# Kernel optimization log

Hardware: AMD Instinct MI355X
Metric: run time of the kernel (lower is better)

Reference implementation:

```python
import jax, jax.numpy as jnp
import numpy as np

# Canonical topology: root object with K arrays, each array has L number leaves.
# Weights are tied across paths (tie_weights_containers=tie_weights_primitives=True),
# NumberEmbedder runs in eval mode with initial buffers mean=0, sqmean=1 -> identity norm.

K, L, D = 8192, 128, 64


def setup_inputs() -> dict:
    key = jax.random.key(0)
    ks = jax.random.split(key, 16)
    s = 1.0 / np.sqrt(D)
    return {
        "x": jax.random.normal(ks[0], (K, L), dtype=jnp.float32),
        "W_num": jax.random.normal(ks[1], (D, 1), dtype=jnp.float32) * s,
        "b_num": jax.random.normal(ks[2], (D,), dtype=jnp.float32) * s,
        "W_ih": jax.random.normal(ks[3], (4 * D, 2 * D), dtype=jnp.float32) * s,
        "W_hh": jax.random.normal(ks[4], (4 * D, D), dtype=jnp.float32) * s,
        "b_ih": jax.random.normal(ks[5], (4 * D,), dtype=jnp.float32) * s,
        "b_hh": jax.random.normal(ks[6], (4 * D,), dtype=jnp.float32) * s,
        "W_aout": jax.random.normal(ks[7], (D, D), dtype=jnp.float32) * s,
        "b_aout": jax.random.normal(ks[8], (D,), dtype=jnp.float32) * s,
        "W_fh": jax.random.normal(ks[9], (D, D), dtype=jnp.float32) * s,
        "b_fh": jax.random.normal(ks[10], (D,), dtype=jnp.float32) * s,
        "W_iouh": jax.random.normal(ks[11], (3 * D, D), dtype=jnp.float32) * s,
        "b_iouh": jax.random.normal(ks[12], (3 * D,), dtype=jnp.float32) * s,
        "W_oout": jax.random.normal(ks[13], (D, D), dtype=jnp.float32) * s,
        "b_oout": jax.random.normal(ks[14], (D,), dtype=jnp.float32) * s,
    }


def _forward(x, W_num, b_num, W_ih, W_hh, b_ih, b_hh, W_aout, b_aout,
             W_fh, b_fh, W_iouh, b_iouh, W_oout, b_oout):
    d = W_hh.shape[1]
    # --- NumberEmbedder: Linear(1, d) on identity-normalized numbers; c = 0 ---
    emb = x[..., None] * W_num[:, 0] + b_num          # [K, L, d]
    xs = jnp.transpose(emb, (1, 0, 2))                # [L, K, d] time-major for scan
    # --- ArrayEmbedder: LSTMCell over children; input = cat(child_h, child_c) ---
    # child_c is identically zero, so only the first half of W_ih contributes.
    W_ih_h = W_ih[:, :d]                              # [4d, d]
    bias = b_ih + b_hh                                # [4d]

    def step(carry, x_t):
        h, c = carry
        gates = x_t @ W_ih_h.T + h @ W_hh.T + bias    # [K, 4d]
        i, f, g, o = jnp.split(gates, 4, axis=1)
        c2 = jax.nn.sigmoid(f) * c + jax.nn.sigmoid(i) * jnp.tanh(g)
        h2 = jax.nn.sigmoid(o) * jnp.tanh(c2)
        return (h2, c2), None

    h0 = jnp.zeros((x.shape[0], d), dtype=x.dtype)
    (h_arr, c_arr), _ = jax.lax.scan(step, (h0, h0), xs)
    h_hat = h_arr @ W_aout.T + b_aout                 # [K, d] array lout
    # --- ObjectEmbedder: child-sum TreeLSTM over the K array states ---
    f = h_hat @ W_fh.T + b_fh                         # [K, d]
    fc_sum = jnp.sum(jax.nn.sigmoid(f) * c_arr, axis=0, keepdims=True)  # [1, d]
    hs_bar = jnp.sum(h_hat, axis=0, keepdims=True)    # [1, d]
    iou = hs_bar @ W_iouh.T + b_iouh                  # [1, 3d]
    i, o, u = jnp.split(iou, 3, axis=1)
    c_obj = jax.nn.sigmoid(i) * jnp.tanh(u) + fc_sum
    h_obj = jax.nn.sigmoid(o) * jnp.tanh(c_obj)
    h_hat_obj = h_obj @ W_oout.T + b_oout             # [1, d] object lout
    # root forward returns cat(h, c)
    return jnp.concatenate([h_hat_obj, c_obj], axis=1)  # [1, 2d]


def reference(x, W_num, b_num, W_ih, W_hh, b_ih, b_hh, W_aout, b_aout,
              W_fh, b_fh, W_iouh, b_iouh, W_oout, b_oout):
    return _forward(x, W_num, b_num, W_ih, W_hh, b_ih, b_hh, W_aout, b_aout,
                    W_fh, b_fh, W_iouh, b_iouh, W_oout, b_oout)
```

## Files before the change

### kernel.cpp

```cpp
#include <hip/hip_runtime.h>
#include <cstddef>

#define D   64
#define L   128
#define NT  256
#define ROWS 16
#define XSS 132
#define HBS 72
#define NBLK 512
#define LOG2E 1.4426950408889634f

typedef __attribute__((ext_vector_type(8))) short short8;
typedef __attribute__((ext_vector_type(4))) float floatx4;
typedef __attribute__((ext_vector_type(2))) float f2;

__device__ __forceinline__ float fast_rcp(float x) {
#if defined(__has_builtin)
#if __has_builtin(__builtin_amdgcn_rcpf)
  return __builtin_amdgcn_rcpf(x);
#else
  return 1.0f / x;
#endif
#else
  return 1.0f / x;
#endif
}
__device__ __forceinline__ float ex2(float x) {
#if defined(__has_builtin)
#if __has_builtin(__builtin_amdgcn_exp2f)
  return __builtin_amdgcn_exp2f(x);
#else
  return __builtin_exp2f(x);
#endif
#else
  return __builtin_exp2f(x);
#endif
}
__device__ __forceinline__ f2 ex2_2(f2 v) { return (f2){ex2(v.x), ex2(v.y)}; }
__device__ __forceinline__ f2 rcp_2(f2 v) { return (f2){fast_rcp(v.x), fast_rcp(v.y)}; }
__device__ __forceinline__ float sig_plain(float x) {
  return fast_rcp(1.0f + ex2(-LOG2E * x));
}
__device__ __forceinline__ float tanh2(float G) {
  return fmaf(2.0f, fast_rcp(1.0f + ex2(G)), -1.0f);
}
__device__ __forceinline__ unsigned short f2bf_rtne(float f) {
  unsigned int u = __float_as_uint(f);
  u += 0x7fffu + ((u >> 16) & 1u);
  return (unsigned short)(u >> 16);
}
__device__ __forceinline__ float bf2f(unsigned short s) {
  return __uint_as_float(((unsigned int)s) << 16);
}

__global__ __launch_bounds__(NT, 2)
void lstm_main(const float* __restrict__ x,
               const float* __restrict__ W_num,
               const float* __restrict__ b_num,
               const float* __restrict__ W_ih,
               const float* __restrict__ W_hh,
               const float* __restrict__ b_ih,
               const float* __restrict__ b_hh,
               const float* __restrict__ W_aout,
               const float* __restrict__ b_aout,
               const float* __restrict__ W_fh,
               const float* __restrict__ b_fh,
               const float* __restrict__ W_iouh,
               const float* __restrict__ b_iouh,
               const float* __restrict__ W_oout,
               const float* __restrict__ b_oout,
               float* __restrict__ acc_out,
               float* __restrict__ out)
{
  __shared__ __align__(16) float xs[ROWS * XSS];
  __shared__ __align__(16) short hb[2][ROWS * HBS];
  __shared__ float sacc[2 * D];
  __shared__ float hobj[D];
  __shared__ int   is_last;

  const int tid  = threadIdx.x;
  const int w    = tid >> 6;
  const int lane = tid & 63;
  const int quad = lane >> 4;
  const int c16  = lane & 15;
  const int k0   = blockIdx.x * ROWS;
  const int dcol = w * 16 + c16;

  for (int i = tid; i < ROWS * (L / 4); i += NT) {
    int r = i >> 5, c4 = i & 31;
    float4 v = ((const float4*)(x + (size_t)(k0 + r) * L))[c4];
    float* dst = &xs[r * XSS + c4 * 4];
    dst[0] = v.x; dst[1] = v.y; dst[2] = v.z; dst[3] = v.w;
  }
  for (int i = tid; i < ROWS * HBS; i += NT) hb[0][i] = 0;

  const float gscale[4] = {-LOG2E, -LOG2E, -2.0f * LOG2E, -LOG2E};

  float An[4], Bc[4];
#pragma unroll
  for (int g = 0; g < 4; ++g) {
    int j = g * 64 + dcol;
    const float4* wr = (const float4*)(W_ih + (size_t)j * (2 * D));
    float a = 0.0f, b = b_ih[j] + b_hh[j];
#pragma unroll
    for (int e4 = 0; e4 < 16; ++e4) {
      float4 wv = wr[e4];
      float4 wn = ((const float4*)W_num)[e4];
      float4 bn = ((const float4*)b_num)[e4];
      a = fmaf(wn.x, wv.x, a); a = fmaf(wn.y, wv.y, a);
      a = fmaf(wn.z, wv.z, a); a = fmaf(wn.w, wv.w, a);
      b = fmaf(bn.x, wv.x, b); b = fmaf(bn.y, wv.y, b);
      b = fmaf(bn.z, wv.z, b); b = fmaf(bn.w, wv.w, b);
    }
    An[g] = a * gscale[g]; Bc[g] = b * gscale[g];
  }

  short8 Bf[4][2];
#pragma unroll
  for (int g = 0; g < 4; ++g) {
#pragma unroll
    for (int kk = 0; kk < 2; ++kk) {
      const float4* wp = (const float4*)(W_hh + (size_t)(g * 64 + dcol) * D
                                         + kk * 32 + quad * 8);
      float wv[8];
      float4 w0 = wp[0], w1 = wp[1];
      wv[0]=w0.x; wv[1]=w0.y; wv[2]=w0.z; wv[3]=w0.w;
      wv[4]=w1.x; wv[5]=w1.y; wv[6]=w1.z; wv[7]=w1.w;
      short8 hi8;
#pragma unroll
      for (int j = 0; j < 8; ++j)
        hi8[j] = (short)f2bf_rtne(wv[j] * gscale[g]);
      Bf[g][kk] = hi8;
    }
  }

  const f2 one2  = {1.0f, 1.0f};
  const f2 m2l2  = {-2.0f * LOG2E, -2.0f * LOG2E};
  f2 creg2[2] = {{0.f, 0.f}, {0.f, 0.f}};
  f2 hreg2[2] = {{0.f, 0.f}, {0.f, 0.f}};
  __syncthreads();

  int p = 0;
  for (int t4 = 0; t4 < L; t4 += 4) {
    float4 xq[4];
#pragma unroll
    for (int r = 0; r < 4; ++r)
      xq[r] = *(const float4*)&xs[(quad * 4 + r) * XSS + t4];
#pragma unroll
    for (int u = 0; u < 4; ++u) {
      short8 ahi[2];
#pragma unroll
      for (int kk = 0; kk < 2; ++kk)
        ahi[kk] = *(const short8*)&hb[p][c16 * HBS + kk * 32 + quad * 8];
      f2 xv01 = {xq[0][u], xq[1][u]};
      f2 xv23 = {xq[2][u], xq[3][u]};
      floatx4 acc[4];
#pragma unroll
      for (int g = 0; g < 4; ++g) {
        f2 A2 = {An[g], An[g]}, B2 = {Bc[g], Bc[g]};
        f2 i01 = A2 * xv01 + B2;
        f2 i23 = A2 * xv23 + B2;
        acc[g] = (floatx4){i01.x, i01.y, i23.x, i23.y};
      }
#pragma unroll
      for (int kk = 0; kk < 2; ++kk) {
#pragma unroll
        for (int g = 0; g < 4; ++g)
          acc[g] = __builtin_amdgcn_mfma_f32_16x16x32_bf16(ahi[kk], Bf[g][kk], acc[g], 0, 0, 0);
      }
#pragma unroll
      for (int h = 0; h < 2; ++h) {
        f2 Gi = {acc[0][2*h], acc[0][2*h+1]};
        f2 Gf = {acc[1][2*h], acc[1][2*h+1]};
        f2 Gg = {acc[2][2*h], acc[2][2*h+1]};
        f2 Go = {acc[3][2*h], acc[3][2*h+1]};
        f2 Ei = ex2_2(Gi), Ef = ex2_2(Gf), Eg = ex2_2(Gg), Eo = ex2_2(Go);
        f2 pf = Ef + one2, pi = Ei + one2, pg = Eg + one2, mg = one2 - Eg;
        f2 pig = pi * pg;
        f2 num = creg2[h] * pig + mg * pf;
        f2 c2  = num * rcp_2(pf * pig);
        creg2[h] = c2;
        f2 Ec = ex2_2(c2 * m2l2);
        f2 po = Eo + one2, pc = Ec + one2, mc = one2 - Ec;
        f2 h2 = mc * rcp_2(po * pc);
        hreg2[h] = h2;
        int row0 = quad * 4 + 2 * h;
        hb[p ^ 1][row0 * HBS + dcol]       = (short)f2bf_rtne(h2.x);
        hb[p ^ 1][(row0 + 1) * HBS + dcol] = (short)f2bf_rtne(h2.y);
      }
      __syncthreads();
      p ^= 1;
    }
  }

  float creg[4] = {creg2[0].x, creg2[0].y, creg2[1].x, creg2[1].y};
  float hreg[4] = {hreg2[0].x, hreg2[0].y, hreg2[1].x, hreg2[1].y};

#pragma unroll
  for (int r = 0; r < 4; ++r) xs[(quad * 4 + r) * XSS + dcol] = hreg[r];
  __syncthreads();

  float hhat[4];
#pragma unroll
  for (int r = 0; r < 4; ++r) {
    float a = b_aout[dcol];
    const float4* wa = (const float4*)(W_aout + (size_t)dcol * D);
    const float* hp = &xs[(quad * 4 + r) * XSS];
#pragma unroll
    for (int e4 = 0; e4 < 16; ++e4) {
      float4 wv = wa[e4];
      a = fmaf(wv.x, hp[e4*4+0], a); a = fmaf(wv.y, hp[e4*4+1], a);
      a = fmaf(wv.z, hp[e4*4+2], a); a = fmaf(wv.w, hp[e4*4+3], a);
    }
    hhat[r] = a;
  }
  __syncthreads();
#pragma unroll
  for (int r = 0; r < 4; ++r) xs[(quad * 4 + r) * XSS + 64 + dcol] = hhat[r];
  __syncthreads();

  float pfc = 0.0f, phs = 0.0f;
#pragma unroll
  for (int r = 0; r < 4; ++r) {
    float f = b_fh[dcol];
    const float4* wf = (const float4*)(W_fh + (size_t)dcol * D);
    const float* hp = &xs[(quad * 4 + r) * XSS + 64];
#pragma unroll
    for (int e4 = 0; e4 < 16; ++e4) {
      float4 wv = wf[e4];
      f = fmaf(wv.x, hp[e4*4+0], f); f = fmaf(wv.y, hp[e4*4+1], f);
      f = fmaf(wv.z, hp[e4*4+2], f); f = fmaf(wv.w, hp[e4*4+3], f);
    }
    pfc = fmaf(sig_plain(f), creg[r], pfc);
    phs += hhat[r];
  }
  pfc += __shfl_xor(pfc, 16); pfc += __shfl_xor(pfc, 32);
  phs += __shfl_xor(phs, 16); phs += __shfl_xor(phs, 32);
  if (quad == 0) {
    atomicAdd(acc_out + dcol, pfc);
    atomicAdd(acc_out + D + dcol, phs);
  }

  __threadfence();
  if (tid == 0) {
    unsigned int prev = __hip_atomic_fetch_add((unsigned int*)(acc_out + 2 * D), 1u,
                                               __ATOMIC_ACQ_REL, __HIP_MEMORY_SCOPE_AGENT);
    is_last = (prev == NBLK - 1) ? 1 : 0;
  }
  __syncthreads();
  if (!is_last) return;
  __threadfence();
  if (tid < 2 * D)
    sacc[tid] = __hip_atomic_load(acc_out + tid, __ATOMIC_RELAXED, __HIP_MEMORY_SCOPE_AGENT);
  __syncthreads();
  if (tid < D) {
    const int d = tid;
    float vi = b_iouh[d], vo = b_iouh[D + d], vu = b_iouh[2 * D + d];
    for (int e = 0; e < D; ++e) {
      float hs = sacc[D + e];
      vi = fmaf(W_iouh[(size_t)d * D + e],           hs, vi);
      vo = fmaf(W_iouh[(size_t)(D + d) * D + e],     hs, vo);
      vu = fmaf(W_iouh[(size_t)(2 * D + d) * D + e], hs, vu);
    }
    float c_obj = sig_plain(vi) * tanh2(-2.0f * LOG2E * vu) + sacc[d];
    float h_obj = sig_plain(vo) * tanh2(-2.0f * LOG2E * c_obj);
    hobj[d] = h_obj;
    out[D + d] = c_obj;
  }
  __syncthreads();
  if (tid < D) {
    const int d = tid;
    float hh = b_oout[d];
    for (int e = 0; e < D; ++e) hh = fmaf(W_oout[(size_t)d * D + e], hobj[e], hh);
    out[d] = hh;
  }
}

extern "C" void kernel_launch(void* const* d_in, const int* in_sizes, int n_in,
                              void* d_out, int out_size, void* d_ws, size_t ws_size,
                              hipStream_t stream) {
  const float* x      = (const float*)d_in[0];
  const float* W_num  = (const float*)d_in[1];
  const float* b_num  = (const float*)d_in[2];
  const float* W_ih   = (const float*)d_in[3];
  const float* W_hh   = (const float*)d_in[4];
  const float* b_ih   = (const float*)d_in[5];
  const float* b_hh   = (const float*)d_in[6];
  const float* W_aout = (const float*)d_in[7];
  const float* b_aout = (const float*)d_in[8];
  const float* W_fh   = (const float*)d_in[9];
  const float* b_fh   = (const float*)d_in[10];
  const float* W_iouh = (const float*)d_in[11];
  const float* b_iouh = (const float*)d_in[12];
  const float* W_oout = (const float*)d_in[13];
  const float* b_oout = (const float*)d_in[14];
  float* acc = (float*)d_ws;
  float* out = (float*)d_out;

  hipMemsetAsync(d_ws, 0, (2 * D + 1) * sizeof(float), stream);
  lstm_main<<<NBLK, NT, 0, stream>>>(x, W_num, b_num, W_ih, W_hh, b_ih, b_hh,
                                     W_aout, b_aout, W_fh, b_fh,
                                     W_iouh, b_iouh, W_oout, b_oout, acc, out);
}
```

Baseline: 202.3 us.

## Halve block to two waves, each computing two 16-column tiles

The block shrinks from 256 to 128 threads, so each wave now owns 32 hidden columns instead of 16. It keeps twice the W_hh fragments and accumulators and issues 8 independent MFMAs per k-slice. The aim is to make each per-timestep __syncthreads cheaper with fewer waves, and to raise instruction-level parallelism so MFMA and transcendental latency in the serial recurrence is hidden. In exchange each wave carries more registers and serial elementwise work. Occupancy per SIMD may also change, so latency hiding across waves could drop.

```diff
diff --git a/kernel.cpp b/kernel.cpp
--- a/kernel.cpp
+++ b/kernel.cpp
@@ -3,7 +3,7 @@
 
 #define D   64
 #define L   128
-#define NT  256
+#define NT  128
 #define ROWS 16
 #define XSS 132
 #define HBS 72
@@ -53,7 +53,7 @@
   return __uint_as_float(((unsigned int)s) << 16);
 }
 
-__global__ __launch_bounds__(NT, 2)
+__global__ __launch_bounds__(NT, 1)
 void lstm_main(const float* __restrict__ x,
                const float* __restrict__ W_num,
                const float* __restrict__ b_num,
@@ -84,7 +84,6 @@
   const int quad = lane >> 4;
   const int c16  = lane & 15;
   const int k0   = blockIdx.x * ROWS;
-  const int dcol = w * 16 + c16;
 
   for (int i = tid; i < ROWS * (L / 4); i += NT) {
     int r = i >> 5, c4 = i & 31;
@@ -96,48 +95,55 @@
 
   const float gscale[4] = {-LOG2E, -LOG2E, -2.0f * LOG2E, -LOG2E};
 
-  float An[4], Bc[4];
-#pragma unroll
-  for (int g = 0; g < 4; ++g) {
-    int j = g * 64 + dcol;
-    const float4* wr = (const float4*)(W_ih + (size_t)j * (2 * D));
-    float a = 0.0f, b = b_ih[j] + b_hh[j];
-#pragma unroll
-    for (int e4 = 0; e4 < 16; ++e4) {
-      float4 wv = wr[e4];
-      float4 wn = ((const float4*)W_num)[e4];
-      float4 bn = ((const float4*)b_num)[e4];
-      a = fmaf(wn.x, wv.x, a); a = fmaf(wn.y, wv.y, a);
-      a = fmaf(wn.z, wv.z, a); a = fmaf(wn.w, wv.w, a);
-      b = fmaf(bn.x, wv.x, b); b = fmaf(bn.y, wv.y, b);
-      b = fmaf(bn.z, wv.z, b); b = fmaf(bn.w, wv.w, b);
-    }
-    An[g] = a * gscale[g]; Bc[g] = b * gscale[g];
-  }
-
-  short8 Bf[4][2];
-#pragma unroll
-  for (int g = 0; g < 4; ++g) {
-#pragma unroll
-    for (int kk = 0; kk < 2; ++kk) {
-      const float4* wp = (const float4*)(W_hh + (size_t)(g * 64 + dcol) * D
-                                         + kk * 32 + quad * 8);
-      float wv[8];
-      float4 w0 = wp[0], w1 = wp[1];
-      wv[0]=w0.x; wv[1]=w0.y; wv[2]=w0.z; wv[3]=w0.w;
-      wv[4]=w1.x; wv[5]=w1.y; wv[6]=w1.z; wv[7]=w1.w;
-      short8 hi8;
-#pragma unroll
-      for (int j = 0; j < 8; ++j)
-        hi8[j] = (short)f2bf_rtne(wv[j] * gscale[g]);
-      Bf[g][kk] = hi8;
+  float An[2][4], Bc[2][4];
+#pragma unroll
+  for (int ct = 0; ct < 2; ++ct) {
+#pragma unroll
+    for (int g = 0; g < 4; ++g) {
+      int j = g * 64 + w * 32 + ct * 16 + c16;
+      const float4* wr = (const float4*)(W_ih + (size_t)j * (2 * D));
+      float a = 0.0f, b = b_ih[j] + b_hh[j];
+#pragma unroll
+      for (int e4 = 0; e4 < 16; ++e4) {
+        float4 wv = wr[e4];
+        float4 wn = ((const float4*)W_num)[e4];
+        float4 bn = ((const float4*)b_num)[e4];
+        a = fmaf(wn.x, wv.x, a); a = fmaf(wn.y, wv.y, a);
+        a = fmaf(wn.z, wv.z, a); a = fmaf(wn.w, wv.w, a);
+        b = fmaf(bn.x, wv.x, b); b = fmaf(bn.y, wv.y, b);
+        b = fmaf(bn.z, wv.z, b); b = fmaf(bn.w, wv.w, b);
+      }
+      An[ct][g] = a * gscale[g]; Bc[ct][g] = b * gscale[g];
+    }
+  }
+
+  short8 Bf[2][4][2];
+#pragma unroll
+  for (int ct = 0; ct < 2; ++ct) {
+#pragma unroll
+    for (int g = 0; g < 4; ++g) {
+#pragma unroll
+      for (int kk = 0; kk < 2; ++kk) {
+        const float4* wp = (const float4*)(W_hh
+                           + (size_t)(g * 64 + w * 32 + ct * 16 + c16) * D
+                           + kk * 32 + quad * 8);
+        float wv[8];
+        float4 w0 = wp[0], w1 = wp[1];
+        wv[0]=w0.x; wv[1]=w0.y; wv[2]=w0.z; wv[3]=w0.w;
+        wv[4]=w1.x; wv[5]=w1.y; wv[6]=w1.z; wv[7]=w1.w;
+        short8 hi8;
+#pragma unroll
+        for (int j = 0; j < 8; ++j)
+          hi8[j] = (short)f2bf_rtne(wv[j] * gscale[g]);
+        Bf[ct][g][kk] = hi8;
+      }
     }
   }
 
   const f2 one2  = {1.0f, 1.0f};
   const f2 m2l2  = {-2.0f * LOG2E, -2.0f * LOG2E};
-  f2 creg2[2] = {{0.f, 0.f}, {0.f, 0.f}};
-  f2 hreg2[2] = {{0.f, 0.f}, {0.f, 0.f}};
+  f2 creg2[2][2] = {{{0.f,0.f},{0.f,0.f}}, {{0.f,0.f},{0.f,0.f}}};
+  f2 hreg2[2][2] = {{{0.f,0.f},{0.f,0.f}}, {{0.f,0.f},{0.f,0.f}}};
   __syncthreads();
 
   int p = 0;
@@ -154,91 +160,131 @@
         ahi[kk] = *(const short8*)&hb[p][c16 * HBS + kk * 32 + quad * 8];
       f2 xv01 = {xq[0][u], xq[1][u]};
       f2 xv23 = {xq[2][u], xq[3][u]};
-      floatx4 acc[4];
-#pragma unroll
-      for (int g = 0; g < 4; ++g) {
-        f2 A2 = {An[g], An[g]}, B2 = {Bc[g], Bc[g]};
-        f2 i01 = A2 * xv01 + B2;
-        f2 i23 = A2 * xv23 + B2;
-        acc[g] = (floatx4){i01.x, i01.y, i23.x, i23.y};
+      floatx4 acc[2][4];
+#pragma unroll
+      for (int ct = 0; ct < 2; ++ct) {
+#pragma unroll
+        for (int g = 0; g < 4; ++g) {
+          f2 A2 = {An[ct][g], An[ct][g]}, B2 = {Bc[ct][g], Bc[ct][g]};
+          f2 i01 = A2 * xv01 + B2;
+          f2 i23 = A2 * xv23 + B2;
+          acc[ct][g] = (floatx4){i01.x, i01.y, i23.x, i23.y};
+        }
       }
 #pragma unroll
       for (int kk = 0; kk < 2; ++kk) {
 #pragma unroll
-        for (int g = 0; g < 4; ++g)
-          acc[g] = __builtin_amdgcn_mfma_f32_16x16x32_bf16(ahi[kk], Bf[g][kk], acc[g], 0, 0, 0);
-      }
-#pragma unroll
-      for (int h = 0; h < 2; ++h) {
-        f2 Gi = {acc[0][2*h], acc[0][2*h+1]};
-        f2 Gf = {acc[1][2*h], acc[1][2*h+1]};
-        f2 Gg = {acc[2][2*h], acc[2][2*h+1]};
-        f2 Go = {acc[3][2*h], acc[3][2*h+1]};
-        f2 Ei = ex2_2(Gi), Ef = ex2_2(Gf), Eg = ex2_2(Gg), Eo = ex2_2(Go);
-        f2 pf = Ef + one2, pi = Ei + one2, pg = Eg + one2, mg = one2 - Eg;
-        f2 pig = pi * pg;
-        f2 num = creg2[h] * pig + mg * pf;
-        f2 c2  = num * rcp_2(pf * pig);
-        creg2[h] = c2;
-        f2 Ec = ex2_2(c2 * m2l2);
-        f2 po = Eo + one2, pc = Ec + one2, mc = one2 - Ec;
-        f2 h2 = mc * rcp_2(po * pc);
-        hreg2[h] = h2;
-        int row0 = quad * 4 + 2 * h;
-        hb[p ^ 1][row0 * HBS + dcol]       = (short)f2bf_rtne(h2.x);
-        hb[p ^ 1][(row0 + 1) * HBS + dcol] = (short)f2bf_rtne(h2.y);
+        for (int ct = 0; ct < 2; ++ct) {
+#pragma unroll
+          for (int g = 0; g < 4; ++g)
+            acc[ct][g] = __builtin_amdgcn_mfma_f32_16x16x32_bf16(
+                           ahi[kk], Bf[ct][g][kk], acc[ct][g], 0, 0, 0);
+        }
+      }
+#pragma unroll
+      for (int ct = 0; ct < 2; ++ct) {
+        const int dcol = w * 32 + ct * 16 + c16;
+#pragma unroll
+        for (int h = 0; h < 2; ++h) {
+          f2 Gi = {acc[ct][0][2*h], acc[ct][0][2*h+1]};
+          f2 Gf = {acc[ct][1][2*h], acc[ct][1][2*h+1]};
+          f2 Gg = {acc[ct][2][2*h], acc[ct][2][2*h+1]};
+          f2 Go = {acc[ct][3][2*h], acc[ct][3][2*h+1]};
+          f2 Ei = ex2_2(Gi), Ef = ex2_2(Gf), Eg = ex2_2(Gg), Eo = ex2_2(Go);
+          f2 pf = Ef + one2, pi = Ei + one2, pg = Eg + one2, mg = one2 - Eg;
+          f2 pig = pi * pg;
+          f2 num = creg2[ct][h] * pig + mg * pf;
+          f2 c2  = num * rcp_2(pf * pig);
+          creg2[ct][h] = c2;
+          f2 Ec = ex2_2(c2 * m2l2);
+          f2 po = Eo + one2, pc = Ec + one2, mc = one2 - Ec;
+          f2 h2 = mc * rcp_2(po * pc);
+          hreg2[ct][h] = h2;
+          int row0 = quad * 4 + 2 * h;
+          hb[p ^ 1][row0 * HBS + dcol]       = (short)f2bf_rtne(h2.x);
+          hb[p ^ 1][(row0 + 1) * HBS + dcol] = (short)f2bf_rtne(h2.y);
+        }
       }
       __syncthreads();
       p ^= 1;
     }
   }
 
-  float creg[4] = {creg2[0].x, creg2[0].y, creg2[1].x, creg2[1].y};
-  float hreg[4] = {hreg2[0].x, hreg2[0].y, hreg2[1].x, hreg2[1].y};
-
-#pragma unroll
-  for (int r = 0; r < 4; ++r) xs[(quad * 4 + r) * XSS + dcol] = hreg[r];
-  __syncthreads();
-
-  float hhat[4];
-#pragma unroll
-  for (int r = 0; r < 4; ++r) {
-    float a = b_aout[dcol];
-    const float4* wa = (const float4*)(W_aout + (size_t)dcol * D);
-    const float* hp = &xs[(quad * 4 + r) * XSS];
-#pragma unroll
-    for (int e4 = 0; e4 < 16; ++e4) {
-      float4 wv = wa[e4];
-      a = fmaf(wv.x, hp[e4*4+0], a); a = fmaf(wv.y, hp[e4*4+1], a);
-      a = fmaf(wv.z, hp[e4*4+2], a); a = fmaf(wv.w, hp[e4*4+3], a);
-    }
-    hhat[r] = a;
-  }
-  __syncthreads();
-#pragma unroll
-  for (int r = 0; r < 4; ++r) xs[(quad * 4 + r) * XSS + 64 + dcol] = hhat[r];
-  __syncthreads();
-
-  float pfc = 0.0f, phs = 0.0f;
-#pragma unroll
-  for (int r = 0; r < 4; ++r) {
-    float f = b_fh[dcol];
-    const float4* wf = (const float4*)(W_fh + (size_t)dcol * D);
-    const float* hp = &xs[(quad * 4 + r) * XSS + 64];
-#pragma unroll
-    for (int e4 = 0; e4 < 16; ++e4) {
-      float4 wv = wf[e4];
-      f = fmaf(wv.x, hp[e4*4+0], f); f = fmaf(wv.y, hp[e4*4+1], f);
-      f = fmaf(wv.z, hp[e4*4+2], f); f = fmaf(wv.w, hp[e4*4+3], f);
-    }
-    pfc = fmaf(sig_plain(f), creg[r], pfc);
-    phs += hhat[r];
-  }
-  pfc += __shfl_xor(pfc, 16); pfc += __shfl_xor(pfc, 32);
-  phs += __shfl_xor(phs, 16); phs += __shfl_xor(phs, 32);
+  float creg[2][4], hreg[2][4];
+#pragma unroll
+  for (int ct = 0; ct < 2; ++ct) {
+    creg[ct][0] = creg2[ct][0].x; creg[ct][1] = creg2[ct][0].y;
+    creg[ct][2] = creg2[ct][1].x; creg[ct][3] = creg2[ct][1].y;
+    hreg[ct][0] = hreg2[ct][0].x; hreg[ct][1] = hreg2[ct][0].y;
+    hreg[ct][2] = hreg2[ct][1].x; hreg[ct][3] = hreg2[ct][1].y;
+  }
+
+#pragma unroll
+  for (int ct = 0; ct < 2; ++ct) {
+    const int dcol = w * 32 + ct * 16 + c16;
+#pragma unroll
+    for (int r = 0; r < 4; ++r) xs[(quad * 4 + r) * XSS + dcol] = hreg[ct][r];
+  }
+  __syncthreads();
+
+  float hhat[2][4];
+#pragma unroll
+  for (int ct = 0; ct < 2; ++ct) {
+    const int dcol = w * 32 + ct * 16 + c16;
+#pragma unroll
+    for (int r = 0; r < 4; ++r) {
+      float a = b_aout[dcol];
+      const float4* wa = (const float4*)(W_aout + (size_t)dcol * D);
+      const float* hp = &xs[(quad * 4 + r) * XSS];
+#pragma unroll
+      for (int e4 = 0; e4 < 16; ++e4) {
+        float4 wv = wa[e4];
+        a = fmaf(wv.x, hp[e4*4+0], a); a = fmaf(wv.y, hp[e4*4+1], a);
+        a = fmaf(wv.z, hp[e4*4+2], a); a = fmaf(wv.w, hp[e4*4+3], a);
+      }
+      hhat[ct][r] = a;
+    }
+  }
+  __syncthreads();
+#pragma unroll
+  for (int ct = 0; ct < 2; ++ct) {
+    const int dcol = w * 32 + ct * 16 + c16;
+#pragma unroll
+    for (int r = 0; r < 4; ++r) xs[(quad * 4 + r) * XSS + 64 + dcol] = hhat[ct][r];
+  }
+  __syncthreads();
+
+  float pfc[2] = {0.0f, 0.0f}, phs[2] = {0.0f, 0.0f};
+#pragma unroll
+  for (int ct = 0; ct < 2; ++ct) {
+    const int dcol = w * 32 + ct * 16 + c16;
+#pragma unroll
+    for (int r = 0; r < 4; ++r) {
+      float f = b_fh[dcol];
+      const float4* wf = (const float4*)(W_fh + (size_t)dcol * D);
+      const float* hp = &xs[(quad * 4 + r) * XSS + 64];
+#pragma unroll
+      for (int e4 = 0; e4 < 16; ++e4) {
+        float4 wv = wf[e4];
+        f = fmaf(wv.x, hp[e4*4+0], f); f = fmaf(wv.y, hp[e4*4+1], f);
+        f = fmaf(wv.z, hp[e4*4+2], f); f = fmaf(wv.w, hp[e4*4+3], f);
+      }
+      pfc[ct] = fmaf(sig_plain(f), creg[ct][r], pfc[ct]);
+      phs[ct] += hhat[ct][r];
+    }
+  }
+#pragma unroll
+  for (int ct = 0; ct < 2; ++ct) {
+    pfc[ct] += __shfl_xor(pfc[ct], 16); pfc[ct] += __shfl_xor(pfc[ct], 32);
+    phs[ct] += __shfl_xor(phs[ct], 16); phs[ct] += __shfl_xor(phs[ct], 32);
+  }
   if (quad == 0) {
-    atomicAdd(acc_out + dcol, pfc);
-    atomicAdd(acc_out + D + dcol, phs);
+#pragma unroll
+    for (int ct = 0; ct < 2; ++ct) {
+      const int dcol = w * 32 + ct * 16 + c16;
+      atomicAdd(acc_out + dcol, pfc[ct]);
+      atomicAdd(acc_out + D + dcol, phs[ct]);
+    }
   }
 
   __threadfence();
```

New measurement: 224.5 us. +11.0%, slower.

## Process two interleaved 16-row tiles per block to hide recurrent latency

Applied to the files above, without the earlier changes.

Each block now handles 32 rows as two independent 16-row LSTM tiles, interleaving their MFMA and transcendental work within each timestep and sharing one barrier per step. The grid halves to 256 blocks and launch bounds drop to one block per SIMD slot. The aim is to fill the serial dependency chain of each recurrence with independent work and amortise barrier cost. In exchange, register pressure rises and the 256-block grid may underfill the GPU's compute units.

```diff
diff --git a/kernel.cpp b/kernel.cpp
--- a/kernel.cpp
+++ b/kernel.cpp
@@ -4,10 +4,11 @@
 #define D   64
 #define L   128
 #define NT  256
-#define ROWS 16
+#define TR  16
+#define ROWS 32
 #define XSS 132
 #define HBS 72
-#define NBLK 512
+#define NBLK 256
 #define LOG2E 1.4426950408889634f
 
 typedef __attribute__((ext_vector_type(8))) short short8;
@@ -49,11 +50,8 @@
   u += 0x7fffu + ((u >> 16) & 1u);
   return (unsigned short)(u >> 16);
 }
-__device__ __forceinline__ float bf2f(unsigned short s) {
-  return __uint_as_float(((unsigned int)s) << 16);
-}
-
-__global__ __launch_bounds__(NT, 2)
+
+__global__ __launch_bounds__(NT, 1)
 void lstm_main(const float* __restrict__ x,
                const float* __restrict__ W_num,
                const float* __restrict__ b_num,
@@ -73,7 +71,7 @@
                float* __restrict__ out)
 {
   __shared__ __align__(16) float xs[ROWS * XSS];
-  __shared__ __align__(16) short hb[2][ROWS * HBS];
+  __shared__ __align__(16) short hb[2][2][TR * HBS];
   __shared__ float sacc[2 * D];
   __shared__ float hobj[D];
   __shared__ int   is_last;
@@ -92,7 +90,7 @@
     float* dst = &xs[r * XSS + c4 * 4];
     dst[0] = v.x; dst[1] = v.y; dst[2] = v.z; dst[3] = v.w;
   }
-  for (int i = tid; i < ROWS * HBS; i += NT) hb[0][i] = 0;
+  for (int i = tid; i < 2 * 2 * TR * HBS; i += NT) ((short*)hb)[i] = 0;
 
   const float gscale[4] = {-LOG2E, -LOG2E, -2.0f * LOG2E, -LOG2E};
 
@@ -136,103 +134,135 @@
 
   const f2 one2  = {1.0f, 1.0f};
   const f2 m2l2  = {-2.0f * LOG2E, -2.0f * LOG2E};
-  f2 creg2[2] = {{0.f, 0.f}, {0.f, 0.f}};
-  f2 hreg2[2] = {{0.f, 0.f}, {0.f, 0.f}};
-  __syncthreads();
+  f2 cregA[2] = {{0.f, 0.f}, {0.f, 0.f}};
+  f2 hregA[2] = {{0.f, 0.f}, {0.f, 0.f}};
+  f2 cregB[2] = {{0.f, 0.f}, {0.f, 0.f}};
+  f2 hregB[2] = {{0.f, 0.f}, {0.f, 0.f}};
+  __syncthreads();
+
+  auto cell_step = [&](const short8 ahi[2], f2 creg2[2], f2 hreg2[2],
+                       f2 xv01, f2 xv23, short* hbw) {
+    floatx4 acc[4];
+#pragma unroll
+    for (int g = 0; g < 4; ++g) {
+      f2 A2 = {An[g], An[g]}, B2 = {Bc[g], Bc[g]};
+      f2 i01 = A2 * xv01 + B2;
+      f2 i23 = A2 * xv23 + B2;
+      acc[g] = (floatx4){i01.x, i01.y, i23.x, i23.y};
+    }
+#pragma unroll
+    for (int kk = 0; kk < 2; ++kk) {
+#pragma unroll
+      for (int g = 0; g < 4; ++g)
+        acc[g] = __builtin_amdgcn_mfma_f32_16x16x32_bf16(ahi[kk], Bf[g][kk], acc[g], 0, 0, 0);
+    }
+#pragma unroll
+    for (int h = 0; h < 2; ++h) {
+      f2 Gi = {acc[0][2*h], acc[0][2*h+1]};
+      f2 Gf = {acc[1][2*h], acc[1][2*h+1]};
+      f2 Gg = {acc[2][2*h], acc[2][2*h+1]};
+      f2 Go = {acc[3][2*h], acc[3][2*h+1]};
+      f2 Ei = ex2_2(Gi), Ef = ex2_2(Gf), Eg = ex2_2(Gg), Eo = ex2_2(Go);
+      f2 pf = Ef + one2, pi = Ei + one2, pg = Eg + one2, mg = one2 - Eg;
+      f2 pig = pi * pg;
+      f2 num = creg2[h] * pig + mg * pf;
+      f2 c2  = num * rcp_2(pf * pig);
+      creg2[h] = c2;
+      f2 Ec = ex2_2(c2 * m2l2);
+      f2 po = Eo + one2, pc = Ec + one2, mc = one2 - Ec;
+      f2 h2 = mc * rcp_2(po * pc);
+      hreg2[h] = h2;
+      int row0 = quad * 4 + 2 * h;
+      hbw[row0 * HBS + dcol]       = (short)f2bf_rtne(h2.x);
+      hbw[(row0 + 1) * HBS + dcol] = (short)f2bf_rtne(h2.y);
+    }
+  };
 
   int p = 0;
   for (int t4 = 0; t4 < L; t4 += 4) {
-    float4 xq[4];
-#pragma unroll
-    for (int r = 0; r < 4; ++r)
-      xq[r] = *(const float4*)&xs[(quad * 4 + r) * XSS + t4];
+    float4 xqA[4], xqB[4];
+#pragma unroll
+    for (int r = 0; r < 4; ++r) {
+      xqA[r] = *(const float4*)&xs[(quad * 4 + r) * XSS + t4];
+      xqB[r] = *(const float4*)&xs[(TR + quad * 4 + r) * XSS + t4];
+    }
 #pragma unroll
     for (int u = 0; u < 4; ++u) {
-      short8 ahi[2];
+      short8 aA[2], aB[2];
 #pragma unroll
       for (int kk = 0; kk < 2; ++kk)
-        ahi[kk] = *(const short8*)&hb[p][c16 * HBS + kk * 32 + quad * 8];
-      f2 xv01 = {xq[0][u], xq[1][u]};
-      f2 xv23 = {xq[2][u], xq[3][u]};
-      floatx4 acc[4];
-#pragma unroll
-      for (int g = 0; g < 4; ++g) {
-        f2 A2 = {An[g], An[g]}, B2 = {Bc[g], Bc[g]};
-        f2 i01 = A2 * xv01 + B2;
-        f2 i23 = A2 * xv23 + B2;
-        acc[g] = (floatx4){i01.x, i01.y, i23.x, i23.y};
-      }
-#pragma unroll
-      for (int kk = 0; kk < 2; ++kk) {
-#pragma unroll
-        for (int g = 0; g < 4; ++g)
-          acc[g] = __builtin_amdgcn_mfma_f32_16x16x32_bf16(ahi[kk], Bf[g][kk], acc[g], 0, 0, 0);
-      }
-#pragma unroll
-      for (int h = 0; h < 2; ++h) {
-        f2 Gi = {acc[0][2*h], acc[0][2*h+1]};
-        f2 Gf = {acc[1][2*h], acc[1][2*h+1]};
-        f2 Gg = {acc[2][2*h], acc[2][2*h+1]};
-        f2 Go = {acc[3][2*h], acc[3][2*h+1]};
-        f2 Ei = ex2_2(Gi), Ef = ex2_2(Gf), Eg = ex2_2(Gg), Eo = ex2_2(Go);
-        f2 pf = Ef + one2, pi = Ei + one2, pg = Eg + one2, mg = one2 - Eg;
-        f2 pig = pi * pg;
-        f2 num = creg2[h] * pig + mg * pf;
-        f2 c2  = num * rcp_2(pf * pig);
-        creg2[h] = c2;
-        f2 Ec = ex2_2(c2 * m2l2);
-        f2 po = Eo + one2, pc = Ec + one2, mc = one2 - Ec;
-        f2 h2 = mc * rcp_2(po * pc);
-        hreg2[h] = h2;
-        int row0 = quad * 4 + 2 * h;
-        hb[p ^ 1][row0 * HBS + dcol]       = (short)f2bf_rtne(h2.x);
-        hb[p ^ 1][(row0 + 1) * HBS + dcol] = (short)f2bf_rtne(h2.y);
-      }
+        aA[kk] = *(const short8*)&hb[0][p][c16 * HBS + kk * 32 + quad * 8];
+#pragma unroll
+      for (int kk = 0; kk < 2; ++kk)
+        aB[kk] = *(const short8*)&hb[1][p][c16 * HBS + kk * 32 + quad * 8];
+
+      f2 xA01 = {xqA[0][u], xqA[1][u]};
+      f2 xA23 = {xqA[2][u], xqA[3][u]};
+      cell_step(aA, cregA, hregA, xA01, xA23, &hb[0][p ^ 1][0]);
+
+      f2 xB01 = {xqB[0][u], xqB[1][u]};
+      f2 xB23 = {xqB[2][u], xqB[3][u]};
+      cell_step(aB, cregB, hregB, xB01, xB23, &hb[1][p ^ 1][0]);
+
       __syncthreads();
       p ^= 1;
     }
   }
 
-  float creg[4] = {creg2[0].x, creg2[0].y, creg2[1].x, creg2[1].y};
-  float hreg[4] = {hreg2[0].x, hreg2[0].y, hreg2[1].x, hreg2[1].y};
-
-#pragma unroll
-  for (int r = 0; r < 4; ++r) xs[(quad * 4 + r) * XSS + dcol] = hreg[r];
-  __syncthreads();
-
-  float hhat[4];
-#pragma unroll
-  for (int r = 0; r < 4; ++r) {
-    float a = b_aout[dcol];
-    const float4* wa = (const float4*)(W_aout + (size_t)dcol * D);
-    const float* hp = &xs[(quad * 4 + r) * XSS];
-#pragma unroll
-    for (int e4 = 0; e4 < 16; ++e4) {
-      float4 wv = wa[e4];
-      a = fmaf(wv.x, hp[e4*4+0], a); a = fmaf(wv.y, hp[e4*4+1], a);
-      a = fmaf(wv.z, hp[e4*4+2], a); a = fmaf(wv.w, hp[e4*4+3], a);
-    }
-    hhat[r] = a;
-  }
-  __syncthreads();
-#pragma unroll
-  for (int r = 0; r < 4; ++r) xs[(quad * 4 + r) * XSS + 64 + dcol] = hhat[r];
+  float creg[2][4] = {{cregA[0].x, cregA[0].y, cregA[1].x, cregA[1].y},
+                      {cregB[0].x, cregB[0].y, cregB[1].x, cregB[1].y}};
+  float hreg[2][4] = {{hregA[0].x, hregA[0].y, hregA[1].x, hregA[1].y},
+                      {hregB[0].x, hregB[0].y, hregB[1].x, hregB[1].y}};
+
+#pragma unroll
+  for (int s = 0; s < 2; ++s)
+#pragma unroll
+    for (int r = 0; r < 4; ++r)
+      xs[(s * TR + quad * 4 + r) * XSS + dcol] = hreg[s][r];
+  __syncthreads();
+
+  float hhat[2][4];
+#pragma unroll
+  for (int s = 0; s < 2; ++s) {
+#pragma unroll
+    for (int r = 0; r < 4; ++r) {
+      float a = b_aout[dcol];
+      const float4* wa = (const float4*)(W_aout + (size_t)dcol * D);
+      const float* hp = &xs[(s * TR + quad * 4 + r) * XSS];
+#pragma unroll
+      for (int e4 = 0; e4 < 16; ++e4) {
+        float4 wv = wa[e4];
+        a = fmaf(wv.x, hp[e4*4+0], a); a = fmaf(wv.y, hp[e4*4+1], a);
+        a = fmaf(wv.z, hp[e4*4+2], a); a = fmaf(wv.w, hp[e4*4+3], a);
+      }
+      hhat[s][r] = a;
+    }
+  }
+  __syncthreads();
+#pragma unroll
+  for (int s = 0; s < 2; ++s)
+#pragma unroll
+    for (int r = 0; r < 4; ++r)
+      xs[(s * TR + quad * 4 + r) * XSS + 64 + dcol] = hhat[s][r];
   __syncthreads();
 
   float pfc = 0.0f, phs = 0.0f;
 #pragma unroll
-  for (int r = 0; r < 4; ++r) {
-    float f = b_fh[dcol];
-    const float4* wf = (const float4*)(W_fh + (size_t)dcol * D);
-    const float* hp = &xs[(quad * 4 + r) * XSS + 64];
-#pragma unroll
-    for (int e4 = 0; e4 < 16; ++e4) {
-      float4 wv = wf[e4];
-      f = fmaf(wv.x, hp[e4*4+0], f); f = fmaf(wv.y, hp[e4*4+1], f);
-      f = fmaf(wv.z, hp[e4*4+2], f); f = fmaf(wv.w, hp[e4*4+3], f);
-    }
-    pfc = fmaf(sig_plain(f), creg[r], pfc);
-    phs += hhat[r];
+  for (int s = 0; s < 2; ++s) {
+#pragma unroll
+    for (int r = 0; r < 4; ++r) {
+      float f = b_fh[dcol];
+      const float4* wf = (const float4*)(W_fh + (size_t)dcol * D);
+      const float* hp = &xs[(s * TR + quad * 4 + r) * XSS + 64];
+#pragma unroll
+      for (int e4 = 0; e4 < 16; ++e4) {
+        float4 wv = wf[e4];
+        f = fmaf(wv.x, hp[e4*4+0], f); f = fmaf(wv.y, hp[e4*4+1], f);
+        f = fmaf(wv.z, hp[e4*4+2], f); f = fmaf(wv.w, hp[e4*4+3], f);
+      }
+      pfc = fmaf(sig_plain(f), creg[s][r], pfc);
+      phs += hhat[s][r];
+    }
   }
   pfc += __shfl_xor(pfc, 16); pfc += __shfl_xor(pfc, 32);
   phs += __shfl_xor(phs, 16); phs += __shfl_xor(phs, 32);
```

Result: slower. 221.3 us (+9.4%).

## Run each 16-row LSTM tile in a single wavefront without per-step barriers

Applied to the files above, without the earlier changes.

Shrinks the block from four waves to one wave that computes all 64 hidden columns (16 MFMA tiles per k-chunk) for its 16 rows. Because only one wave touches the hidden-state buffer, the per-timestep __syncthreads and the double-buffered hb are dropped, and hidden states are written with packed 64-bit LDS stores. The epilogue matvecs and reductions are restructured so each lane handles four columns. In exchange, each wave does four times as much serial MFMA and transcendental work per step. With 512 single-wave blocks, fewer SIMDs per CU may have work to hide latency, and register pressure rises.

```diff
diff --git a/kernel.cpp b/kernel.cpp
--- a/kernel.cpp
+++ b/kernel.cpp
@@ -3,7 +3,7 @@
 
 #define D   64
 #define L   128
-#define NT  256
+#define NT  64
 #define ROWS 16
 #define XSS 132
 #define HBS 72
@@ -49,11 +49,8 @@
   u += 0x7fffu + ((u >> 16) & 1u);
   return (unsigned short)(u >> 16);
 }
-__device__ __forceinline__ float bf2f(unsigned short s) {
-  return __uint_as_float(((unsigned int)s) << 16);
-}
-
-__global__ __launch_bounds__(NT, 2)
+
+__global__ __launch_bounds__(NT, 1)
 void lstm_main(const float* __restrict__ x,
                const float* __restrict__ W_num,
                const float* __restrict__ b_num,
@@ -73,18 +70,16 @@
                float* __restrict__ out)
 {
   __shared__ __align__(16) float xs[ROWS * XSS];
-  __shared__ __align__(16) short hb[2][ROWS * HBS];
+  __shared__ __align__(16) short hb[ROWS * HBS];
   __shared__ float sacc[2 * D];
   __shared__ float hobj[D];
   __shared__ int   is_last;
 
   const int tid  = threadIdx.x;
-  const int w    = tid >> 6;
-  const int lane = tid & 63;
-  const int quad = lane >> 4;
-  const int c16  = lane & 15;
+  const int quad = tid >> 4;
+  const int c16  = tid & 15;
   const int k0   = blockIdx.x * ROWS;
-  const int dcol = w * 16 + c16;
+  const int col0 = 4 * c16;
 
   for (int i = tid; i < ROWS * (L / 4); i += NT) {
     int r = i >> 5, c4 = i & 31;
@@ -92,36 +87,41 @@
     float* dst = &xs[r * XSS + c4 * 4];
     dst[0] = v.x; dst[1] = v.y; dst[2] = v.z; dst[3] = v.w;
   }
-  for (int i = tid; i < ROWS * HBS; i += NT) hb[0][i] = 0;
+  for (int i = tid; i < ROWS * HBS; i += NT) hb[i] = 0;
 
   const float gscale[4] = {-LOG2E, -LOG2E, -2.0f * LOG2E, -LOG2E};
 
-  float An[4], Bc[4];
-#pragma unroll
-  for (int g = 0; g < 4; ++g) {
-    int j = g * 64 + dcol;
+  float4 wn[16], bn[16];
+#pragma unroll
+  for (int e4 = 0; e4 < 16; ++e4) {
+    wn[e4] = ((const float4*)W_num)[e4];
+    bn[e4] = ((const float4*)b_num)[e4];
+  }
+
+  float An[16], Bc[16];
+#pragma unroll
+  for (int t = 0; t < 16; ++t) {
+    int j = (t >> 2) * 64 + col0 + (t & 3);
     const float4* wr = (const float4*)(W_ih + (size_t)j * (2 * D));
     float a = 0.0f, b = b_ih[j] + b_hh[j];
 #pragma unroll
     for (int e4 = 0; e4 < 16; ++e4) {
       float4 wv = wr[e4];
-      float4 wn = ((const float4*)W_num)[e4];
-      float4 bn = ((const float4*)b_num)[e4];
-      a = fmaf(wn.x, wv.x, a); a = fmaf(wn.y, wv.y, a);
-      a = fmaf(wn.z, wv.z, a); a = fmaf(wn.w, wv.w, a);
-      b = fmaf(bn.x, wv.x, b); b = fmaf(bn.y, wv.y, b);
-      b = fmaf(bn.z, wv.z, b); b = fmaf(bn.w, wv.w, b);
-    }
-    An[g] = a * gscale[g]; Bc[g] = b * gscale[g];
-  }
-
-  short8 Bf[4][2];
-#pragma unroll
-  for (int g = 0; g < 4; ++g) {
+      a = fmaf(wn[e4].x, wv.x, a); a = fmaf(wn[e4].y, wv.y, a);
+      a = fmaf(wn[e4].z, wv.z, a); a = fmaf(wn[e4].w, wv.w, a);
+      b = fmaf(bn[e4].x, wv.x, b); b = fmaf(bn[e4].y, wv.y, b);
+      b = fmaf(bn[e4].z, wv.z, b); b = fmaf(bn[e4].w, wv.w, b);
+    }
+    An[t] = a * gscale[t >> 2]; Bc[t] = b * gscale[t >> 2];
+  }
+
+  short8 Bf[16][2];
+#pragma unroll
+  for (int t = 0; t < 16; ++t) {
 #pragma unroll
     for (int kk = 0; kk < 2; ++kk) {
-      const float4* wp = (const float4*)(W_hh + (size_t)(g * 64 + dcol) * D
-                                         + kk * 32 + quad * 8);
+      const float4* wp = (const float4*)(W_hh
+          + (size_t)((t >> 2) * 64 + col0 + (t & 3)) * D + kk * 32 + quad * 8);
       float wv[8];
       float4 w0 = wp[0], w1 = wp[1];
       wv[0]=w0.x; wv[1]=w0.y; wv[2]=w0.z; wv[3]=w0.w;
@@ -129,18 +129,19 @@
       short8 hi8;
 #pragma unroll
       for (int j = 0; j < 8; ++j)
-        hi8[j] = (short)f2bf_rtne(wv[j] * gscale[g]);
-      Bf[g][kk] = hi8;
-    }
-  }
-
-  const f2 one2  = {1.0f, 1.0f};
-  const f2 m2l2  = {-2.0f * LOG2E, -2.0f * LOG2E};
-  f2 creg2[2] = {{0.f, 0.f}, {0.f, 0.f}};
-  f2 hreg2[2] = {{0.f, 0.f}, {0.f, 0.f}};
-  __syncthreads();
-
-  int p = 0;
+        hi8[j] = (short)f2bf_rtne(wv[j] * gscale[t >> 2]);
+      Bf[t][kk] = hi8;
+    }
+  }
+
+  const f2 one2 = {1.0f, 1.0f};
+  const f2 m2l2 = {-2.0f * LOG2E, -2.0f * LOG2E};
+  f2 creg2[4][2] = {{{0.f,0.f},{0.f,0.f}}, {{0.f,0.f},{0.f,0.f}},
+                    {{0.f,0.f},{0.f,0.f}}, {{0.f,0.f},{0.f,0.f}}};
+  f2 hreg2[4][2] = {{{0.f,0.f},{0.f,0.f}}, {{0.f,0.f},{0.f,0.f}},
+                    {{0.f,0.f},{0.f,0.f}}, {{0.f,0.f},{0.f,0.f}}};
+  __syncthreads();
+
   for (int t4 = 0; t4 < L; t4 += 4) {
     float4 xq[4];
 #pragma unroll
@@ -151,94 +152,125 @@
       short8 ahi[2];
 #pragma unroll
       for (int kk = 0; kk < 2; ++kk)
-        ahi[kk] = *(const short8*)&hb[p][c16 * HBS + kk * 32 + quad * 8];
+        ahi[kk] = *(const short8*)&hb[c16 * HBS + kk * 32 + quad * 8];
       f2 xv01 = {xq[0][u], xq[1][u]};
       f2 xv23 = {xq[2][u], xq[3][u]};
-      floatx4 acc[4];
-#pragma unroll
-      for (int g = 0; g < 4; ++g) {
-        f2 A2 = {An[g], An[g]}, B2 = {Bc[g], Bc[g]};
+      floatx4 acc[16];
+#pragma unroll
+      for (int t = 0; t < 16; ++t) {
+        f2 A2 = {An[t], An[t]}, B2 = {Bc[t], Bc[t]};
         f2 i01 = A2 * xv01 + B2;
         f2 i23 = A2 * xv23 + B2;
-        acc[g] = (floatx4){i01.x, i01.y, i23.x, i23.y};
+        acc[t] = (floatx4){i01.x, i01.y, i23.x, i23.y};
       }
 #pragma unroll
       for (int kk = 0; kk < 2; ++kk) {
 #pragma unroll
-        for (int g = 0; g < 4; ++g)
-          acc[g] = __builtin_amdgcn_mfma_f32_16x16x32_bf16(ahi[kk], Bf[g][kk], acc[g], 0, 0, 0);
-      }
-#pragma unroll
-      for (int h = 0; h < 2; ++h) {
-        f2 Gi = {acc[0][2*h], acc[0][2*h+1]};
-        f2 Gf = {acc[1][2*h], acc[1][2*h+1]};
-        f2 Gg = {acc[2][2*h], acc[2][2*h+1]};
-        f2 Go = {acc[3][2*h], acc[3][2*h+1]};
-        f2 Ei = ex2_2(Gi), Ef = ex2_2(Gf), Eg = ex2_2(Gg), Eo = ex2_2(Go);
-        f2 pf = Ef + one2, pi = Ei + one2, pg = Eg + one2, mg = one2 - Eg;
-        f2 pig = pi * pg;
-        f2 num = creg2[h] * pig + mg * pf;
-        f2 c2  = num * rcp_2(pf * pig);
-        creg2[h] = c2;
-        f2 Ec = ex2_2(c2 * m2l2);
-        f2 po = Eo + one2, pc = Ec + one2, mc = one2 - Ec;
-        f2 h2 = mc * rcp_2(po * pc);
-        hreg2[h] = h2;
-        int row0 = quad * 4 + 2 * h;
-        hb[p ^ 1][row0 * HBS + dcol]       = (short)f2bf_rtne(h2.x);
-        hb[p ^ 1][(row0 + 1) * HBS + dcol] = (short)f2bf_rtne(h2.y);
-      }
-      __syncthreads();
-      p ^= 1;
-    }
-  }
-
-  float creg[4] = {creg2[0].x, creg2[0].y, creg2[1].x, creg2[1].y};
-  float hreg[4] = {hreg2[0].x, hreg2[0].y, hreg2[1].x, hreg2[1].y};
-
-#pragma unroll
-  for (int r = 0; r < 4; ++r) xs[(quad * 4 + r) * XSS + dcol] = hreg[r];
-  __syncthreads();
-
-  float hhat[4];
+        for (int t = 0; t < 16; ++t)
+          acc[t] = __builtin_amdgcn_mfma_f32_16x16x32_bf16(ahi[kk], Bf[t][kk], acc[t], 0, 0, 0);
+      }
+#pragma unroll
+      for (int dt = 0; dt < 4; ++dt) {
+#pragma unroll
+        for (int h = 0; h < 2; ++h) {
+          f2 Gi = {acc[dt][2*h],      acc[dt][2*h+1]};
+          f2 Gf = {acc[4 + dt][2*h],  acc[4 + dt][2*h+1]};
+          f2 Gg = {acc[8 + dt][2*h],  acc[8 + dt][2*h+1]};
+          f2 Go = {acc[12 + dt][2*h], acc[12 + dt][2*h+1]};
+          f2 Ei = ex2_2(Gi), Ef = ex2_2(Gf), Eg = ex2_2(Gg), Eo = ex2_2(Go);
+          f2 pf = Ef + one2, pi = Ei + one2, pg = Eg + one2, mg = one2 - Eg;
+          f2 pig = pi * pg;
+          f2 num = creg2[dt][h] * pig + mg * pf;
+          f2 c2  = num * rcp_2(pf * pig);
+          creg2[dt][h] = c2;
+          f2 Ec = ex2_2(c2 * m2l2);
+          f2 po = Eo + one2, pc = Ec + one2, mc = one2 - Ec;
+          f2 h2 = mc * rcp_2(po * pc);
+          hreg2[dt][h] = h2;
+        }
+      }
+#pragma unroll
+      for (int r = 0; r < 4; ++r) {
+        float h0 = (r & 1) ? hreg2[0][r >> 1].y : hreg2[0][r >> 1].x;
+        float h1 = (r & 1) ? hreg2[1][r >> 1].y : hreg2[1][r >> 1].x;
+        float h2v = (r & 1) ? hreg2[2][r >> 1].y : hreg2[2][r >> 1].x;
+        float h3 = (r & 1) ? hreg2[3][r >> 1].y : hreg2[3][r >> 1].x;
+        unsigned int b0 = (unsigned int)f2bf_rtne(h0) | ((unsigned int)f2bf_rtne(h1) << 16);
+        unsigned int b1 = (unsigned int)f2bf_rtne(h2v) | ((unsigned int)f2bf_rtne(h3) << 16);
+        unsigned long long wv = (unsigned long long)b0 | ((unsigned long long)b1 << 32);
+        *(unsigned long long*)(&hb[(quad * 4 + r) * HBS + col0]) = wv;
+      }
+    }
+  }
+
 #pragma unroll
   for (int r = 0; r < 4; ++r) {
-    float a = b_aout[dcol];
-    const float4* wa = (const float4*)(W_aout + (size_t)dcol * D);
-    const float* hp = &xs[(quad * 4 + r) * XSS];
-#pragma unroll
-    for (int e4 = 0; e4 < 16; ++e4) {
-      float4 wv = wa[e4];
-      a = fmaf(wv.x, hp[e4*4+0], a); a = fmaf(wv.y, hp[e4*4+1], a);
-      a = fmaf(wv.z, hp[e4*4+2], a); a = fmaf(wv.w, hp[e4*4+3], a);
-    }
-    hhat[r] = a;
-  }
-  __syncthreads();
-#pragma unroll
-  for (int r = 0; r < 4; ++r) xs[(quad * 4 + r) * XSS + 64 + dcol] = hhat[r];
-  __syncthreads();
-
-  float pfc = 0.0f, phs = 0.0f;
+    float4 hv;
+    hv.x = (r & 1) ? hreg2[0][r >> 1].y : hreg2[0][r >> 1].x;
+    hv.y = (r & 1) ? hreg2[1][r >> 1].y : hreg2[1][r >> 1].x;
+    hv.z = (r & 1) ? hreg2[2][r >> 1].y : hreg2[2][r >> 1].x;
+    hv.w = (r & 1) ? hreg2[3][r >> 1].y : hreg2[3][r >> 1].x;
+    *(float4*)&xs[(quad * 4 + r) * XSS + col0] = hv;
+  }
+  __syncthreads();
+
+  float hhat[4][4];
+#pragma unroll
+  for (int dt = 0; dt < 4; ++dt) {
+    const int col = col0 + dt;
+    const float4* wa = (const float4*)(W_aout + (size_t)col * D);
+#pragma unroll
+    for (int r = 0; r < 4; ++r) {
+      float a = b_aout[col];
+      const float* hp = &xs[(quad * 4 + r) * XSS];
+#pragma unroll
+      for (int e4 = 0; e4 < 16; ++e4) {
+        float4 wv = wa[e4];
+        a = fmaf(wv.x, hp[e4*4+0], a); a = fmaf(wv.y, hp[e4*4+1], a);
+        a = fmaf(wv.z, hp[e4*4+2], a); a = fmaf(wv.w, hp[e4*4+3], a);
+      }
+      hhat[r][dt] = a;
+    }
+  }
+  __syncthreads();
 #pragma unroll
   for (int r = 0; r < 4; ++r) {
-    float f = b_fh[dcol];
-    const float4* wf = (const float4*)(W_fh + (size_t)dcol * D);
-    const float* hp = &xs[(quad * 4 + r) * XSS + 64];
-#pragma unroll
-    for (int e4 = 0; e4 < 16; ++e4) {
-      float4 wv = wf[e4];
-      f = fmaf(wv.x, hp[e4*4+0], f); f = fmaf(wv.y, hp[e4*4+1], f);
-      f = fmaf(wv.z, hp[e4*4+2], f); f = fmaf(wv.w, hp[e4*4+3], f);
-    }
-    pfc = fmaf(sig_plain(f), creg[r], pfc);
-    phs += hhat[r];
-  }
-  pfc += __shfl_xor(pfc, 16); pfc += __shfl_xor(pfc, 32);
-  phs += __shfl_xor(phs, 16); phs += __shfl_xor(phs, 32);
+    float4 hv = {hhat[r][0], hhat[r][1], hhat[r][2], hhat[r][3]};
+    *(float4*)&xs[(quad * 4 + r) * XSS + 64 + col0] = hv;
+  }
+  __syncthreads();
+
+  float pfc[4] = {0.f, 0.f, 0.f, 0.f}, phs[4] = {0.f, 0.f, 0.f, 0.f};
+#pragma unroll
+  for (int dt = 0; dt < 4; ++dt) {
+    const int col = col0 + dt;
+    const float4* wf = (const float4*)(W_fh + (size_t)col * D);
+#pragma unroll
+    for (int r = 0; r < 4; ++r) {
+      float f = b_fh[col];
+      const float* hp = &xs[(quad * 4 + r) * XSS + 64];
+#pragma unroll
+      for (int e4 = 0; e4 < 16; ++e4) {
+        float4 wv = wf[e4];
+        f = fmaf(wv.x, hp[e4*4+0], f); f = fmaf(wv.y, hp[e4*4+1], f);
+        f = fmaf(wv.z, hp[e4*4+2], f); f = fmaf(wv.w, hp[e4*4+3], f);
+      }
+      float cv = (r & 1) ? creg2[dt][r >> 1].y : creg2[dt][r >> 1].x;
+      pfc[dt] = fmaf(sig_plain(f), cv, pfc[dt]);
+      phs[dt] += hhat[r][dt];
+    }
+  }
+#pragma unroll
+  for (int dt = 0; dt < 4; ++dt) {
+    pfc[dt] += __shfl_xor(pfc[dt], 16); pfc[dt] += __shfl_xor(pfc[dt], 32);
+    phs[dt] += __shfl_xor(phs[dt], 16); phs[dt] += __shfl_xor(phs[dt], 32);
+  }
   if (quad == 0) {
-    atomicAdd(acc_out + dcol, pfc);
-    atomicAdd(acc_out + D + dcol, phs);
+#pragma unroll
+    for (int dt = 0; dt < 4; ++dt) {
+      atomicAdd(acc_out + col0 + dt, pfc[dt]);
+      atomicAdd(acc_out + D + col0 + dt, phs[dt]);
+    }
   }
 
   __threadfence();
@@ -250,10 +282,10 @@
   __syncthreads();
   if (!is_last) return;
   __threadfence();
-  if (tid < 2 * D)
-    sacc[tid] = __hip_atomic_load(acc_out + tid, __ATOMIC_RELAXED, __HIP_MEMORY_SCOPE_AGENT);
-  __syncthreads();
-  if (tid < D) {
+  for (int i = tid; i < 2 * D; i += NT)
+    sacc[i] = __hip_atomic_load(acc_out + i, __ATOMIC_RELAXED, __HIP_MEMORY_SCOPE_AGENT);
+  __syncthreads();
+  {
     const int d = tid;
     float vi = b_iouh[d], vo = b_iouh[D + d], vu = b_iouh[2 * D + d];
     for (int e = 0; e < D; ++e) {
@@ -268,7 +300,7 @@
     out[D + d] = c_obj;
   }
   __syncthreads();
-  if (tid < D) {
+  {
     const int d = tid;
     float hh = b_oout[d];
     for (int e = 0; e < D; ++e) hh = fmaf(W_oout[(size_t)d * D + e], hobj[e], hh);
```

Measured after the change: 339.7 us. 67.9% more time.
